# Kernel optimization log

Measured on AMD Instinct MI355X. Metric: run time of the kernel, lower is better.

## Reference

```python
import jax, jax.numpy as jnp
import numpy as np

VOCAB = 128000
HID = 128
OUT = 5
N_TREES = 16
N_LEAVES = 64


def _build_trees():
    # Post-order (children before parent) node arrays for N_TREES balanced
    # binary trees; indices are global across the whole batch of trees.
    is_leaf, left, right = [], [], []
    def rec(nl):
        if nl == 1:
            i = len(is_leaf)
            is_leaf.append(True); left.append(i); right.append(i)
            return i
        l = rec(nl // 2)
        r = rec(nl - nl // 2)
        i = len(is_leaf)
        is_leaf.append(False); left.append(l); right.append(r)
        return i
    for _ in range(N_TREES):
        rec(N_LEAVES)
    return (np.array(is_leaf), np.array(left, np.int64), np.array(right, np.int64))


def setup_inputs() -> dict:
    key = jax.random.key(0)
    ks = jax.random.split(key, 8)
    il, l, r = _build_trees()
    n = il.shape[0]  # 2032
    word_idx = jax.random.randint(ks[0], (n,), 0, VOCAB)
    s = 0.05  # scale randn params so tanh does not fully saturate
    return {
        "embed": jax.random.normal(ks[1], (VOCAB, HID), jnp.float32) * s,
        "V": jax.random.normal(ks[2], (HID, 2 * HID, 2 * HID), jnp.float32) * s,
        "W": jax.random.normal(ks[3], (2 * HID, HID), jnp.float32) * s,
        "b": jax.random.normal(ks[4], (1, HID), jnp.float32) * s,
        "Wout_w": jax.random.normal(ks[5], (HID, OUT), jnp.float32) * s,
        "Wout_b": jax.random.normal(ks[6], (OUT,), jnp.float32) * s,
        "is_leaf": jnp.asarray(il),
        "word_idx": word_idx,
        "left_idx": jnp.asarray(l),
        "right_idx": jnp.asarray(r),
    }


def _forward(embed, V, W, b, Wout_w, Wout_b, is_leaf, word_idx, left_idx, right_idx):
    n = is_leaf.shape[0]
    h = W.shape[1]

    def step(Hs, xs):
        i, lf, w, l, r = xs
        c = jnp.concatenate([Hs[l], Hs[r]])              # [2h] concat of children
        xVx = jnp.einsum('k,hkl,l->h', c, V, c)          # bilinear V term, one scalar per slice
        internal = jnp.tanh(xVx + c @ W + b[0])          # [h]
        cur = jnp.where(lf, embed[w], internal)          # leaf -> embedding lookup
        return Hs.at[i].set(cur), None

    H0 = jnp.zeros((n, h), dtype=embed.dtype)
    Hs, _ = jax.lax.scan(
        step, H0,
        (jnp.arange(n), is_leaf, word_idx, left_idx, right_idx))
    # all-node output (root_only=False): log_softmax(W_out(h))
    return jax.nn.log_softmax(Hs @ Wout_w + Wout_b, axis=1)


def reference(embed, V, W, b, Wout_w, Wout_b, is_leaf, word_idx, left_idx, right_idx):
    return _forward(embed, V, W, b, Wout_w, Wout_b,
                    is_leaf, word_idx, left_idx, right_idx)
```

## Files before the change

### kernel.cpp

```cpp
#include <hip/hip_runtime.h>

#define HID 128
#define NODES 2032
#define NPT 127
#define NW 1024

typedef _Float16 f16x8 __attribute__((ext_vector_type(8)));
typedef _Float16 f16x4 __attribute__((ext_vector_type(4)));
typedef float f32x4 __attribute__((ext_vector_type(4)));

__device__ __forceinline__ int tree_idx(int p, int sst) {
  return (p + 1) * sst + p - __popc(p) - 1;
}
__device__ __forceinline__ int cswz(int row, int colbyte) {
  return row * 512 + (colbyte ^ ((row & 31) << 4));
}

__device__ __forceinline__ unsigned int cload(const void* p) {
  return __hip_atomic_load((const unsigned int*)p, __ATOMIC_RELAXED, __HIP_MEMORY_SCOPE_AGENT);
}
__device__ __forceinline__ void cstore(void* p, unsigned int v) {
  __hip_atomic_store((unsigned int*)p, v, __ATOMIC_RELAXED, __HIP_MEMORY_SCOPE_AGENT);
}
__device__ __forceinline__ float cloadf(const void* p) {
  union { unsigned int u; float f; } c; c.u = cload(p); return c.f;
}
__device__ __forceinline__ void cstoref(void* p, float f) {
  union { float f; unsigned int u; } c; c.f = f; cstore(p, c.u);
}

__device__ __forceinline__ void gbar(int* sb, int ph) {
  asm volatile("s_waitcnt vmcnt(0)" ::: "memory");
  __syncthreads();
  if (threadIdx.x == 0) {
    int* base = sb + ph * 1024;
    const int grp = blockIdx.x & 15;
    int v = __hip_atomic_fetch_add(base + grp * 32, 1, __ATOMIC_RELAXED, __HIP_MEMORY_SCOPE_AGENT);
    if (v == 15) {
      int r = __hip_atomic_fetch_add(base + 768, 1, __ATOMIC_RELAXED, __HIP_MEMORY_SCOPE_AGENT);
      if (r == 15)
        __hip_atomic_store(base + 800, 1, __ATOMIC_RELAXED, __HIP_MEMORY_SCOPE_AGENT);
    }
    while (!__hip_atomic_load(base + 800, __ATOMIC_RELAXED, __HIP_MEMORY_SCOPE_AGENT))
      __builtin_amdgcn_s_sleep(4);
  }
  __syncthreads();
}

__global__ __launch_bounds__(512, 1) void rntn_kernel(
    const float* __restrict__ V, const float* __restrict__ W, const float* __restrict__ bb,
    const float* __restrict__ embed, const int* __restrict__ word_idx,
    const float* __restrict__ Wout, const float* __restrict__ Wb,
    _Float16* __restrict__ H16A, _Float16* __restrict__ H16B,
    float* __restrict__ Hgt, float* __restrict__ out, int* __restrict__ syncb)
{
  __shared__ _Float16 Alds[256 * 256];
  __shared__ _Float16 Ct[32 * 256];
  __shared__ float red[8][32];

  const int bid = blockIdx.x;
  const int h = bid >> 1, part = bid & 1;
  const int tid = threadIdx.x, lane = tid & 63, w = tid >> 6;
  const int lo16 = lane & 15, q = lane >> 4;
  const int nidx = tid & 31, oct = tid >> 5;
  const int r8 = tid >> 3, seg = tid & 7;
  char* ab = (char*)Alds;
  char* cb = (char*)Ct;

  float4 ef0, ef1, ef2, ef3;
  {
    const int nodeL = r8 >> 1, child = r8 & 1;
    const int lp = 2 * (part * 256 + nodeL) + child;
    const int tt = lp >> 6, pp = lp & 63;
    const int g = tt * NPT + 2 * pp - __popc(pp);
    const int wi = word_idx[g];
    const float* src = embed + (size_t)wi * HID + seg * 16;
    ef0 = ((const float4*)src)[0]; ef1 = ((const float4*)src)[1];
    ef2 = ((const float4*)src)[2]; ef3 = ((const float4*)src)[3];
  }

  {
    const int arow = tid >> 1, ahalf = tid & 1;
    const float* src = V + (size_t)h * 65536 + (size_t)arow * 256 + ahalf * 128;
#pragma unroll
    for (int u2 = 0; u2 < 16; ++u2) {
      const float4 a = ((const float4*)src)[u2 * 2];
      const float4 b2 = ((const float4*)src)[u2 * 2 + 1];
      f16x8 v;
      v[0] = (_Float16)a.x;  v[1] = (_Float16)a.y;
      v[2] = (_Float16)a.z;  v[3] = (_Float16)a.w;
      v[4] = (_Float16)b2.x; v[5] = (_Float16)b2.y;
      v[6] = (_Float16)b2.z; v[7] = (_Float16)b2.w;
      *(f16x8*)(ab + cswz(arow, ahalf * 256 + u2 * 16)) = v;
    }
  }
  f32x4 wk[2];
#pragma unroll
  for (int rf = 0; rf < 2; ++rf) {
    const int kb = w * 32 + rf * 16 + q * 4;
#pragma unroll
    for (int i = 0; i < 4; ++i)
      wk[rf][i] = W[(size_t)(kb + i) * HID + h];
  }
  const float bh = bb[h];
  __syncthreads();

  for (int lv = 0; lv < 6; ++lv) {
    const int m = 512 >> lv;
    const int lognpt = 5 - lv;
    const int sst = (1 << (lv + 2)) - 1;
    _Float16* Hp = (lv & 1) ? H16A : H16B;
    _Float16* Hn = (lv & 1) ? H16B : H16A;
    const int nodes_blk = m >> 1;
    const int n_start = part * nodes_blk;
    const int ntiles = (nodes_blk + 31) >> 5;

    unsigned int u[8];
    if (lv > 0) {
      const int nn0 = nodes_blk > 32 ? 32 : nodes_blk;
      if (nidx < nn0) {
#pragma unroll
        for (int j = 0; j < 8; ++j)
          u[j] = cload(Hp + (size_t)(oct * 8 + j) * NW + 2 * (n_start + nidx));
      }
    }

    for (int t = 0; t < ntiles; ++t) {
      const int nb = n_start + t * 32;
      int nn = nodes_blk - t * 32; if (nn > 32) nn = 32;
      const int ncf = (nn + 15) >> 4;

      __syncthreads();
      if (lv == 0) {
        f16x8 v0, v1;
        v0[0] = (_Float16)ef0.x; v0[1] = (_Float16)ef0.y;
        v0[2] = (_Float16)ef0.z; v0[3] = (_Float16)ef0.w;
        v0[4] = (_Float16)ef1.x; v0[5] = (_Float16)ef1.y;
        v0[6] = (_Float16)ef1.z; v0[7] = (_Float16)ef1.w;
        v1[0] = (_Float16)ef2.x; v1[1] = (_Float16)ef2.y;
        v1[2] = (_Float16)ef2.z; v1[3] = (_Float16)ef2.w;
        v1[4] = (_Float16)ef3.x; v1[5] = (_Float16)ef3.y;
        v1[6] = (_Float16)ef3.z; v1[7] = (_Float16)ef3.w;
        const int nodeL = r8 >> 1, child = r8 & 1;
        *(f16x8*)(cb + cswz(nodeL, child * 256 + seg * 32)) = v0;
        *(f16x8*)(cb + cswz(nodeL, child * 256 + seg * 32 + 16)) = v1;
      } else {
        if (nidx < nn) {
          union { f16x8 v; unsigned short s[8]; } a0, a1;
#pragma unroll
          for (int j = 0; j < 8; ++j) {
            a0.s[j] = (unsigned short)(u[j] & 0xffffu);
            a1.s[j] = (unsigned short)(u[j] >> 16);
          }
          *(f16x8*)(cb + cswz(nidx, oct * 16)) = a0.v;
          *(f16x8*)(cb + cswz(nidx, 256 + oct * 16)) = a1.v;
        }
      }
      __syncthreads();

      if (t + 1 < ntiles) {
        if (lv == 0) {
          const int nodeL = r8 >> 1, child = r8 & 1;
          const int lp = 2 * (nb + 32 + nodeL) + child;
          const int tt = lp >> 6, pp = lp & 63;
          const int g = tt * NPT + 2 * pp - __popc(pp);
          const int wi = word_idx[g];
          const float* src = embed + (size_t)wi * HID + seg * 16;
          ef0 = ((const float4*)src)[0]; ef1 = ((const float4*)src)[1];
          ef2 = ((const float4*)src)[2]; ef3 = ((const float4*)src)[3];
        } else {
          int nnn = nodes_blk - (t + 1) * 32; if (nnn > 32) nnn = 32;
          if (nidx < nnn) {
#pragma unroll
            for (int j = 0; j < 8; ++j)
              u[j] = cload(Hp + (size_t)(oct * 8 + j) * NW + 2 * (nb + 32 + nidx));
          }
        }
      }

      f32x4 acc[2][2];
#pragma unroll
      for (int rf = 0; rf < 2; ++rf)
#pragma unroll
        for (int cf = 0; cf < 2; ++cf) { f32x4 z = {0.f, 0.f, 0.f, 0.f}; acc[rf][cf] = z; }

#pragma unroll
      for (int lc = 0; lc < 8; ++lc) {
        f16x8 Af[2];
#pragma unroll
        for (int rf = 0; rf < 2; ++rf)
          Af[rf] = *(const f16x8*)(ab + cswz(w * 32 + rf * 16 + lo16, lc * 64 + q * 16));
#pragma unroll
        for (int cf = 0; cf < 2; ++cf) {
          if (cf < ncf) {
            const int nl = cf * 16 + lo16;
            const f16x8 Bf = *(const f16x8*)(cb + cswz(nl, lc * 64 + q * 16));
#pragma unroll
            for (int rf = 0; rf < 2; ++rf)
              acc[rf][cf] = __builtin_amdgcn_mfma_f32_16x16x32_f16(Af[rf], Bf, acc[rf][cf], 0, 0, 0);
          }
        }
      }

      float pt[2];
#pragma unroll
      for (int cf = 0; cf < 2; ++cf) {
        pt[cf] = 0.f;
        if (cf < ncf) {
          const int nl = cf * 16 + lo16;
          float s = 0.f;
#pragma unroll
          for (int rf = 0; rf < 2; ++rf) {
            const int kb = w * 32 + rf * 16 + q * 4;
            const f16x4 cv = *(const f16x4*)(cb + cswz(nl, kb * 2));
            s += (float)cv[0] * (acc[rf][cf][0] + wk[rf][0])
               + (float)cv[1] * (acc[rf][cf][1] + wk[rf][1])
               + (float)cv[2] * (acc[rf][cf][2] + wk[rf][2])
               + (float)cv[3] * (acc[rf][cf][3] + wk[rf][3]);
          }
          pt[cf] = s;
        }
      }
#pragma unroll
      for (int cf = 0; cf < 2; ++cf) {
        pt[cf] += __shfl_xor(pt[cf], 16);
        pt[cf] += __shfl_xor(pt[cf], 32);
      }
      if (q == 0) {
#pragma unroll
        for (int cf = 0; cf < 2; ++cf)
          if (cf < ncf) red[w][cf * 16 + lo16] = pt[cf];
      }
      __syncthreads();

      if (tid < (nn >> 1)) {
        float x0 = bh, x1 = bh;
#pragma unroll
        for (int ww = 0; ww < 8; ++ww) {
          x0 += red[ww][2 * tid];
          x1 += red[ww][2 * tid + 1];
        }
        const float t0 = tanhf(x0), t1 = tanhf(x1);
        union { _Float16 f; unsigned short s; } c0, c1;
        c0.f = (_Float16)t0; c1.f = (_Float16)t1;
        const int n0 = nb + 2 * tid;
        cstore(Hn + (size_t)h * NW + n0, (unsigned)c0.s | ((unsigned)c1.s << 16));
        const int mask = (1 << lognpt) - 1;
        const int g0 = ((n0) >> lognpt) * NPT + tree_idx(n0 & mask, sst);
        const int g1 = ((n0 + 1) >> lognpt) * NPT + tree_idx((n0 + 1) & mask, sst);
        cstoref(Hgt + (size_t)h * 2048 + g0, t0);
        cstoref(Hgt + (size_t)h * 2048 + g1, t1);
      }
      if (lv == 0 && tid < 2 * nn) {
        const int nodeL = tid >> 1, child = tid & 1;
        const int lp = 2 * (nb + nodeL) + child;
        const int tt = lp >> 6, pp = lp & 63;
        const int g = tt * NPT + 2 * pp - __popc(pp);
        const _Float16 hv = *(const _Float16*)(cb + cswz(nodeL, child * 256 + 2 * h));
        cstoref(Hgt + (size_t)h * 2048 + g, (float)hv);
      }
    }
    gbar(syncb, lv);
  }

  if (bid < 127 && tid < 256) {
    const int node = bid * 16 + (tid >> 4);
    const int hs = tid & 15;
    float l0 = 0.f, l1 = 0.f, l2 = 0.f, l3 = 0.f, l4 = 0.f;
#pragma unroll
    for (int j = 0; j < 8; ++j) {
      const int hh = hs + j * 16;
      const float x = cloadf(Hgt + (size_t)hh * 2048 + node);
      const float* wr = Wout + (size_t)hh * 5;
      l0 += x * wr[0]; l1 += x * wr[1]; l2 += x * wr[2];
      l3 += x * wr[3]; l4 += x * wr[4];
    }
#pragma unroll
    for (int d = 1; d < 16; d <<= 1) {
      l0 += __shfl_xor(l0, d); l1 += __shfl_xor(l1, d); l2 += __shfl_xor(l2, d);
      l3 += __shfl_xor(l3, d); l4 += __shfl_xor(l4, d);
    }
    if (hs == 0) {
      l0 += Wb[0]; l1 += Wb[1]; l2 += Wb[2]; l3 += Wb[3]; l4 += Wb[4];
      const float mm = fmaxf(fmaxf(fmaxf(l0, l1), fmaxf(l2, l3)), l4);
      const float ss = expf(l0 - mm) + expf(l1 - mm) + expf(l2 - mm)
                     + expf(l3 - mm) + expf(l4 - mm);
      const float lse = mm + logf(ss);
      float* o = out + (size_t)node * 5;
      o[0] = l0 - lse; o[1] = l1 - lse; o[2] = l2 - lse; o[3] = l3 - lse; o[4] = l4 - lse;
    }
  }
}

extern "C" void kernel_launch(void* const* d_in, const int* in_sizes, int n_in,
                              void* d_out, int out_size, void* d_ws, size_t ws_size,
                              hipStream_t stream) {
  const float* embed = (const float*)d_in[0];
  const float* V     = (const float*)d_in[1];
  const float* W     = (const float*)d_in[2];
  const float* b     = (const float*)d_in[3];
  const float* Wout  = (const float*)d_in[4];
  const float* Woutb = (const float*)d_in[5];
  const int* word_idx = (const int*)d_in[7];
  float* out = (float*)d_out;

  char* wsb = (char*)d_ws;
  _Float16* H16A = (_Float16*)wsb;
  _Float16* H16B = (_Float16*)(wsb + 262144);
  float*    Hgt  = (float*)(wsb + 524288);
  int*     syncb = (int*)(wsb + 1572864);

  hipMemsetAsync(syncb, 0, 32768, stream);
  rntn_kernel<<<256, 512, 0, stream>>>(V, W, b, embed, word_idx, Wout, Woutb,
                                       H16A, H16B, Hgt, out, syncb);
}
```

Baseline: 76.41 us.

## Restructure tile staging loop, spread barrier release flags, write leaf embeddings from registers

After: 71.51 us, median of 2. 1.07x faster.

```diff
diff --git a/kernel.cpp b/kernel.cpp
--- a/kernel.cpp
+++ b/kernel.cpp
@@ -14,6 +14,14 @@
 }
 __device__ __forceinline__ int cswz(int row, int colbyte) {
   return row * 512 + (colbyte ^ ((row & 31) << 4));
+}
+__device__ __forceinline__ float pick16(float4 a, float4 b, float4 c, float4 d, int i) {
+  float4 s0x = (i & 8) ? c : a;
+  float4 s1x = (i & 8) ? d : b;
+  float4 s = (i & 4) ? s1x : s0x;
+  float lo = (i & 1) ? s.y : s.x;
+  float hi = (i & 1) ? s.w : s.z;
+  return (i & 2) ? hi : lo;
 }
 
 __device__ __forceinline__ unsigned int cload(const void* p) {
@@ -38,10 +46,13 @@
     int v = __hip_atomic_fetch_add(base + grp * 32, 1, __ATOMIC_RELAXED, __HIP_MEMORY_SCOPE_AGENT);
     if (v == 15) {
       int r = __hip_atomic_fetch_add(base + 768, 1, __ATOMIC_RELAXED, __HIP_MEMORY_SCOPE_AGENT);
-      if (r == 15)
-        __hip_atomic_store(base + 800, 1, __ATOMIC_RELAXED, __HIP_MEMORY_SCOPE_AGENT);
-    }
-    while (!__hip_atomic_load(base + 800, __ATOMIC_RELAXED, __HIP_MEMORY_SCOPE_AGENT))
+      if (r == 15) {
+#pragma unroll
+        for (int gg = 0; gg < 16; ++gg)
+          __hip_atomic_store(base + 512 + gg * 16, 1, __ATOMIC_RELAXED, __HIP_MEMORY_SCOPE_AGENT);
+      }
+    }
+    while (!__hip_atomic_load(base + 512 + grp * 16, __ATOMIC_RELAXED, __HIP_MEMORY_SCOPE_AGENT))
       __builtin_amdgcn_s_sleep(4);
   }
   __syncthreads();
@@ -64,6 +75,7 @@
   const int lo16 = lane & 15, q = lane >> 4;
   const int nidx = tid & 31, oct = tid >> 5;
   const int r8 = tid >> 3, seg = tid & 7;
+  const int hseg = h >> 4, hcomp = h & 15;
   char* ab = (char*)Alds;
   char* cb = (char*)Ct;
 
@@ -103,7 +115,6 @@
       wk[rf][i] = W[(size_t)(kb + i) * HID + h];
   }
   const float bh = bb[h];
-  __syncthreads();
 
   for (int lv = 0; lv < 6; ++lv) {
     const int m = 512 >> lv;
@@ -116,47 +127,48 @@
     const int ntiles = (nodes_blk + 31) >> 5;
 
     unsigned int u[8];
-    if (lv > 0) {
+    if (lv == 0) {
+      const int nodeL = r8 >> 1, child = r8 & 1;
+      f16x8 v0, v1;
+      v0[0] = (_Float16)ef0.x; v0[1] = (_Float16)ef0.y;
+      v0[2] = (_Float16)ef0.z; v0[3] = (_Float16)ef0.w;
+      v0[4] = (_Float16)ef1.x; v0[5] = (_Float16)ef1.y;
+      v0[6] = (_Float16)ef1.z; v0[7] = (_Float16)ef1.w;
+      v1[0] = (_Float16)ef2.x; v1[1] = (_Float16)ef2.y;
+      v1[2] = (_Float16)ef2.z; v1[3] = (_Float16)ef2.w;
+      v1[4] = (_Float16)ef3.x; v1[5] = (_Float16)ef3.y;
+      v1[6] = (_Float16)ef3.z; v1[7] = (_Float16)ef3.w;
+      *(f16x8*)(cb + cswz(nodeL, child * 256 + seg * 32)) = v0;
+      *(f16x8*)(cb + cswz(nodeL, child * 256 + seg * 32 + 16)) = v1;
+      if (seg == hseg) {
+        const int lp = 2 * (n_start + nodeL) + child;
+        const int tt = lp >> 6, pp = lp & 63;
+        const int g = tt * NPT + 2 * pp - __popc(pp);
+        cstoref(Hgt + (size_t)h * 2048 + g, pick16(ef0, ef1, ef2, ef3, hcomp));
+      }
+    } else {
       const int nn0 = nodes_blk > 32 ? 32 : nodes_blk;
       if (nidx < nn0) {
 #pragma unroll
         for (int j = 0; j < 8; ++j)
           u[j] = cload(Hp + (size_t)(oct * 8 + j) * NW + 2 * (n_start + nidx));
-      }
-    }
+        union { f16x8 v; unsigned short s[8]; } a0, a1;
+#pragma unroll
+        for (int j = 0; j < 8; ++j) {
+          a0.s[j] = (unsigned short)(u[j] & 0xffffu);
+          a1.s[j] = (unsigned short)(u[j] >> 16);
+        }
+        *(f16x8*)(cb + cswz(nidx, oct * 16)) = a0.v;
+        *(f16x8*)(cb + cswz(nidx, 256 + oct * 16)) = a1.v;
+      }
+    }
+    __syncthreads();
 
     for (int t = 0; t < ntiles; ++t) {
       const int nb = n_start + t * 32;
       int nn = nodes_blk - t * 32; if (nn > 32) nn = 32;
       const int ncf = (nn + 15) >> 4;
-
-      __syncthreads();
-      if (lv == 0) {
-        f16x8 v0, v1;
-        v0[0] = (_Float16)ef0.x; v0[1] = (_Float16)ef0.y;
-        v0[2] = (_Float16)ef0.z; v0[3] = (_Float16)ef0.w;
-        v0[4] = (_Float16)ef1.x; v0[5] = (_Float16)ef1.y;
-        v0[6] = (_Float16)ef1.z; v0[7] = (_Float16)ef1.w;
-        v1[0] = (_Float16)ef2.x; v1[1] = (_Float16)ef2.y;
-        v1[2] = (_Float16)ef2.z; v1[3] = (_Float16)ef2.w;
-        v1[4] = (_Float16)ef3.x; v1[5] = (_Float16)ef3.y;
-        v1[6] = (_Float16)ef3.z; v1[7] = (_Float16)ef3.w;
-        const int nodeL = r8 >> 1, child = r8 & 1;
-        *(f16x8*)(cb + cswz(nodeL, child * 256 + seg * 32)) = v0;
-        *(f16x8*)(cb + cswz(nodeL, child * 256 + seg * 32 + 16)) = v1;
-      } else {
-        if (nidx < nn) {
-          union { f16x8 v; unsigned short s[8]; } a0, a1;
-#pragma unroll
-          for (int j = 0; j < 8; ++j) {
-            a0.s[j] = (unsigned short)(u[j] & 0xffffu);
-            a1.s[j] = (unsigned short)(u[j] >> 16);
-          }
-          *(f16x8*)(cb + cswz(nidx, oct * 16)) = a0.v;
-          *(f16x8*)(cb + cswz(nidx, 256 + oct * 16)) = a1.v;
-        }
-      }
-      __syncthreads();
+      int nnn = nodes_blk - (t + 1) * 32; if (nnn > 32) nnn = 32;
 
       if (t + 1 < ntiles) {
         if (lv == 0) {
@@ -169,7 +181,6 @@
           ef0 = ((const float4*)src)[0]; ef1 = ((const float4*)src)[1];
           ef2 = ((const float4*)src)[2]; ef3 = ((const float4*)src)[3];
         } else {
-          int nnn = nodes_blk - (t + 1) * 32; if (nnn > 32) nnn = 32;
           if (nidx < nnn) {
 #pragma unroll
             for (int j = 0; j < 8; ++j)
@@ -251,14 +262,40 @@
         cstoref(Hgt + (size_t)h * 2048 + g0, t0);
         cstoref(Hgt + (size_t)h * 2048 + g1, t1);
       }
-      if (lv == 0 && tid < 2 * nn) {
-        const int nodeL = tid >> 1, child = tid & 1;
-        const int lp = 2 * (nb + nodeL) + child;
-        const int tt = lp >> 6, pp = lp & 63;
-        const int g = tt * NPT + 2 * pp - __popc(pp);
-        const _Float16 hv = *(const _Float16*)(cb + cswz(nodeL, child * 256 + 2 * h));
-        cstoref(Hgt + (size_t)h * 2048 + g, (float)hv);
-      }
+      if (t + 1 < ntiles) {
+        if (lv == 0) {
+          const int nodeL = r8 >> 1, child = r8 & 1;
+          f16x8 v0, v1;
+          v0[0] = (_Float16)ef0.x; v0[1] = (_Float16)ef0.y;
+          v0[2] = (_Float16)ef0.z; v0[3] = (_Float16)ef0.w;
+          v0[4] = (_Float16)ef1.x; v0[5] = (_Float16)ef1.y;
+          v0[6] = (_Float16)ef1.z; v0[7] = (_Float16)ef1.w;
+          v1[0] = (_Float16)ef2.x; v1[1] = (_Float16)ef2.y;
+          v1[2] = (_Float16)ef2.z; v1[3] = (_Float16)ef2.w;
+          v1[4] = (_Float16)ef3.x; v1[5] = (_Float16)ef3.y;
+          v1[6] = (_Float16)ef3.z; v1[7] = (_Float16)ef3.w;
+          *(f16x8*)(cb + cswz(nodeL, child * 256 + seg * 32)) = v0;
+          *(f16x8*)(cb + cswz(nodeL, child * 256 + seg * 32 + 16)) = v1;
+          if (seg == hseg) {
+            const int lp = 2 * (nb + 32 + nodeL) + child;
+            const int tt = lp >> 6, pp = lp & 63;
+            const int g = tt * NPT + 2 * pp - __popc(pp);
+            cstoref(Hgt + (size_t)h * 2048 + g, pick16(ef0, ef1, ef2, ef3, hcomp));
+          }
+        } else {
+          if (nidx < nnn) {
+            union { f16x8 v; unsigned short s[8]; } a0, a1;
+#pragma unroll
+            for (int j = 0; j < 8; ++j) {
+              a0.s[j] = (unsigned short)(u[j] & 0xffffu);
+              a1.s[j] = (unsigned short)(u[j] >> 16);
+            }
+            *(f16x8*)(cb + cswz(nidx, oct * 16)) = a0.v;
+            *(f16x8*)(cb + cswz(nidx, 256 + oct * 16)) = a1.v;
+          }
+        }
+      }
+      __syncthreads();
     }
     gbar(syncb, lv);
   }
@@ -310,7 +347,7 @@
   float*    Hgt  = (float*)(wsb + 524288);
   int*     syncb = (int*)(wsb + 1572864);
 
-  hipMemsetAsync(syncb, 0, 32768, stream);
+  hipMemsetAsync(syncb, 0, 24576, stream);
   rntn_kernel<<<256, 512, 0, stream>>>(V, W, b, embed, word_idx, Wout, Woutb,
                                        H16A, H16B, Hgt, out, syncb);
 }
```
